# Performance work log

Hardware: AMD Instinct MI355X
Metric: run time of the kernel (lower is better)

Reference implementation:

```python
import jax, jax.numpy as jnp
import numpy as np

B, L, H, E = 2, 2048, 16, 64  # S == L (causal self-attention), D == E


def setup_inputs() -> dict:
    key = jax.random.key(0)
    kq, kk, kv, ks = jax.random.split(key, 4)
    queries = jax.random.normal(kq, (B, L, H, E), dtype=jnp.float32)
    keys = jax.random.normal(kk, (B, L, H, E), dtype=jnp.float32)
    values = jax.random.normal(kv, (B, L, H, E), dtype=jnp.float32)
    # TriangularCausalMask: True above the diagonal -> masked out
    attn_mask = jnp.broadcast_to(
        jnp.triu(jnp.ones((L, L), dtype=bool), k=1)[None, None], (B, 1, L, L)
    )
    init_score = jax.random.uniform(ks, (B, L, L), dtype=jnp.float32)
    return {
        "queries": queries,
        "keys": keys,
        "values": values,
        "attn_mask": attn_mask,
        "init_score": init_score,
    }


def reference(queries, keys, values, attn_mask, init_score):
    # queries: [B,L,H,E], keys: [B,S,H,E], values: [B,S,H,D]
    E_ = queries.shape[-1]
    scale = 1.0 / np.sqrt(E_).astype(np.float32)
    # scores: [B,H,L,S]
    scores = jnp.einsum('blhe,bshe->bhls', queries, keys)
    scores = jnp.where(attn_mask, -jnp.inf, scores)
    A = jax.nn.softmax(scale * scores, axis=-1)  # dropout p=0 -> identity
    # post-softmax bias, broadcast over heads
    A = A + 0.1 * init_score[:, None, :, :]
    # V: [B,L,H,D]
    V = jnp.einsum('bhls,bshd->blhd', A, values)
    return V
```

## Files before the change

kernel.cpp:

```cpp
#include <hip/hip_runtime.h>
#include <hip/hip_bf16.h>
#include <math.h>

#define BB 2
#define LL 2048
#define HH 16
#define EE 64
#define LOG2E 1.44269504089f

typedef __attribute__((ext_vector_type(8))) short short8;
typedef __attribute__((ext_vector_type(4))) float floatx4;
typedef unsigned int u32;

union S8 { short8 v; u32 u[4]; ushort4 q[2]; };

__device__ inline u32 pkbf(float lo, float hi) {
    union { __hip_bfloat162 h; u32 u; } c;
    c.h = __float22bfloat162_rn(make_float2(lo, hi));
    return c.u;
}

__device__ inline ushort4 cvt4(float4 v) {
    union { __hip_bfloat162 h; u32 u; } a, b;
    a.h = __float22bfloat162_rn(make_float2(v.x, v.y));
    b.h = __float22bfloat162_rn(make_float2(v.z, v.w));
    ushort4 r;
    r.x = (unsigned short)(a.u & 0xffffu);
    r.y = (unsigned short)(a.u >> 16);
    r.z = (unsigned short)(b.u & 0xffffu);
    r.w = (unsigned short)(b.u >> 16);
    return r;
}

__device__ inline short8 pack8(float4 a, float4 b) {
    S8 s; s.q[0] = cvt4(a); s.q[1] = cvt4(b); return s.v;
}

__device__ inline void async16(unsigned short* lds, const unsigned short* g) {
    __builtin_amdgcn_global_load_lds(
        (const __attribute__((address_space(1))) u32*)g,
        (__attribute__((address_space(3))) u32*)lds, 16, 0, 0);
}

__global__ __launch_bounds__(256) void prepass(
    const float* __restrict__ k, const float* __restrict__ v,
    const float* __restrict__ isc, unsigned short* __restrict__ kb,
    unsigned short* __restrict__ vt, unsigned short* __restrict__ isb)
{
    const int bid = blockIdx.x;
    const int t = threadIdx.x;
    if (bid < 1024) {
        #pragma unroll
        for (int it = 0; it < 2; ++it) {
            int idx = bid * 512 + it * 256 + t;
            const float4* src = (const float4*)k + idx * 2;
            float4 a = src[0], c = src[1];
            int e8 = idx & 7, h = (idx >> 3) & 15, l = (idx >> 7) & 2047, b = idx >> 18;
            *(short8*)&kb[(((b * 16 + h) * 2048 + l) * 64) + e8 * 8] = pack8(a, c);
        }
    } else if (bid < 2048) {
        const int ib = bid - 1024;
        #pragma unroll
        for (int it = 0; it < 4; ++it) {
            int idx = ib * 1024 + it * 256 + t;
            const float4* src = (const float4*)isc + idx * 2;
            float4 a = src[0], c = src[1];
            a.x *= 0.1f; a.y *= 0.1f; a.z *= 0.1f; a.w *= 0.1f;
            c.x *= 0.1f; c.y *= 0.1f; c.z *= 0.1f; c.w *= 0.1f;
            ((short8*)isb)[idx] = pack8(a, c);
        }
    } else {
        __shared__ float Tf[64][68];
        const int vb = bid - 2048;
        const int st = vb & 31, h = (vb >> 5) & 15, b = vb >> 9;
        const int s0 = st * 64;
        #pragma unroll
        for (int i = 0; i < 4; ++i) {
            int r = i * 16 + (t >> 4), c = (t & 15) * 4;
            float4 val = *(const float4*)(v + (((b * LL + s0 + r) * HH + h) * EE) + c);
            *(float4*)&Tf[r][c] = val;
        }
        __syncthreads();
        #pragma unroll
        for (int i = 0; i < 4; ++i) {
            int d = i * 16 + (t >> 4), s4 = (t & 15) * 4;
            float4 val = make_float4(Tf[s4 + 0][d], Tf[s4 + 1][d],
                                     Tf[s4 + 2][d], Tf[s4 + 3][d]);
            *(ushort4*)&vt[((b * 16 + h) * 64 + d) * 2048 + s0 + s4] = cvt4(val);
        }
    }
}

template <int MODE>
__device__ __forceinline__ void tile_step(
    const unsigned short* __restrict__ Ks, const unsigned short* __restrict__ Vs,
    const short8 qf[2], const short8 isf[2],
    floatx4 o_attn[4], floatx4 o_bias[4], float& lsum,
    int s0, int mbase, int wave, int lq, int ln, int lnl,
    int alo, int ahi, bool hisel)
{
    u32 pk[4][2];
    if (MODE < 2) {
        #pragma unroll
        for (int sb = 0; sb < 4; ++sb) {
            if (MODE == 1 && wave < sb) { pk[sb][0] = 0; pk[sb][1] = 0; continue; }
            short8 kf0 = *(const short8*)&Ks[(sb * 16 + ln) * 64 + ((lq ^ lnl) << 3)];
            short8 kf1 = *(const short8*)&Ks[(sb * 16 + ln) * 64 + (((4 + lq) ^ lnl) << 3)];
            floatx4 sa = {0.f, 0.f, 0.f, 0.f};
            sa = __builtin_amdgcn_mfma_f32_16x16x32_bf16(kf0, qf[0], sa, 0, 0, 0);
            sa = __builtin_amdgcn_mfma_f32_16x16x32_bf16(kf1, qf[1], sa, 0, 0, 0);
            float pv[4];
            #pragma unroll
            for (int r = 0; r < 4; ++r) {
                float t = sa[r];
                if (MODE == 1 && (s0 + sb * 16 + lq * 4 + r) > (mbase + ln)) t = -INFINITY;
                float p = exp2f(t);
                lsum += p;
                pv[r] = p;
            }
            pk[sb][0] = pkbf(pv[0], pv[1]);
            pk[sb][1] = pkbf(pv[2], pv[3]);
        }
    }
    #pragma unroll
    for (int kk = 0; kk < 2; ++kk) {
        short8 vf[4];
        #pragma unroll
        for (int db = 0; db < 4; ++db)
            vf[db] = *(const short8*)&Vs[(db * 16 + ln) * 64 + (((kk * 4 + lq) ^ lnl) << 3)];
        short8 af = isf[kk];
        #pragma unroll
        for (int db = 0; db < 4; ++db)
            o_bias[db] = __builtin_amdgcn_mfma_f32_16x16x32_bf16(af, vf[db], o_bias[db], 0, 0, 0);
        if (MODE < 2) {
            S8 pf;
            u32 a0 = (u32)__builtin_amdgcn_ds_bpermute(alo, (int)pk[kk * 2][0]);
            u32 b0 = (u32)__builtin_amdgcn_ds_bpermute(alo, (int)pk[kk * 2 + 1][0]);
            pf.u[0] = hisel ? b0 : a0;
            u32 a1 = (u32)__builtin_amdgcn_ds_bpermute(alo, (int)pk[kk * 2][1]);
            u32 b1 = (u32)__builtin_amdgcn_ds_bpermute(alo, (int)pk[kk * 2 + 1][1]);
            pf.u[1] = hisel ? b1 : a1;
            u32 a2 = (u32)__builtin_amdgcn_ds_bpermute(ahi, (int)pk[kk * 2][0]);
            u32 b2 = (u32)__builtin_amdgcn_ds_bpermute(ahi, (int)pk[kk * 2 + 1][0]);
            pf.u[2] = hisel ? b2 : a2;
            u32 a3 = (u32)__builtin_amdgcn_ds_bpermute(ahi, (int)pk[kk * 2][1]);
            u32 b3 = (u32)__builtin_amdgcn_ds_bpermute(ahi, (int)pk[kk * 2 + 1][1]);
            pf.u[3] = hisel ? b3 : a3;
            #pragma unroll
            for (int db = 0; db < 4; ++db)
                o_attn[db] = __builtin_amdgcn_mfma_f32_16x16x32_bf16(pf.v, vf[db], o_attn[db], 0, 0, 0);
        }
    }
}

__global__ __launch_bounds__(256, 4) void fused6(
    const float* __restrict__ q, const unsigned short* __restrict__ kb,
    const unsigned short* __restrict__ vt, const unsigned short* __restrict__ isb,
    float* __restrict__ out)
{
    __shared__ unsigned short Ks[2][64 * 64];
    __shared__ unsigned short Vs[2][64 * 64];

    const int tid = threadIdx.x, lane = tid & 63, wave = tid >> 6;
    const int lq = lane >> 4, ln = lane & 15, lnl = ln & 7;

    const int bid = blockIdx.x;
    const int h = bid & 15, b = (bid >> 4) & 1, g = bid >> 5;
    int qt;
    if (g < 8) qt = 31 - g;
    else if (g < 16) qt = g;
    else if (g < 24) qt = 39 - g;
    else qt = g - 24;
    const int q0 = qt * 64;
    const int mbase = q0 + wave * 16;

    short8 qf[2];
    {
        const float sc = 0.125f * LOG2E;
        const float* qrow = q + (((long)(b * LL + mbase + ln)) * HH + h) * EE;
        #pragma unroll
        for (int kk = 0; kk < 2; ++kk) {
            float4 a = *(const float4*)(qrow + kk * 32 + lq * 8);
            float4 c = *(const float4*)(qrow + kk * 32 + lq * 8 + 4);
            a.x *= sc; a.y *= sc; a.z *= sc; a.w *= sc;
            c.x *= sc; c.y *= sc; c.z *= sc; c.w *= sc;
            qf[kk] = pack8(a, c);
        }
    }

    const unsigned short* kbh = kb + (long)(b * HH + h) * (LL * EE);
    const unsigned short* vth = vt + (long)(b * HH + h) * (EE * LL);

    floatx4 o_attn[4], o_bias[4];
    #pragma unroll
    for (int db = 0; db < 4; ++db) {
        o_attn[db] = (floatx4){0.f, 0.f, 0.f, 0.f};
        o_bias[db] = (floatx4){0.f, 0.f, 0.f, 0.f};
    }
    float lsum = 0.f;

    const int rr = lane >> 3, jl = lane & 7;
    const int swz = (jl ^ rr) * 8;
    const unsigned short* ksrc0 = kbh + (wave * 16 + rr) * 64 + swz;
    const unsigned short* ksrc1 = kbh + (wave * 16 + 8 + rr) * 64 + swz;
    const unsigned short* vsrc0 = vth + (wave * 16 + rr) * LL + swz;
    const unsigned short* vsrc1 = vth + (wave * 16 + 8 + rr) * LL + swz;

    const unsigned short* isrow =
        isb + (long)(b * LL + q0 + wave * 16 + ln) * LL + lq * 8;

    const int alo = (((lq & 1) * 2) * 16 + ln) * 4;
    const int ahi = (((lq & 1) * 2 + 1) * 16 + ln) * 4;
    const bool hisel = (lq >= 2);

    auto issue = [&](int j) {
        const int s0 = j * 64, bsel = j & 1;
        if (j <= qt) {
            async16(&Ks[bsel][(wave * 16) * 64], ksrc0 + s0 * 64);
            async16(&Ks[bsel][(wave * 16 + 8) * 64], ksrc1 + s0 * 64);
        }
        async16(&Vs[bsel][(wave * 16) * 64], vsrc0 + s0);
        async16(&Vs[bsel][(wave * 16 + 8) * 64], vsrc1 + s0);
    };

    short8 isf[2], isfn[2];
    auto ldnext = [&](int j, short8* dst) {
        int jc = j < 32 ? j : 31;
        dst[0] = *(const short8*)(isrow + jc * 64);
        dst[1] = *(const short8*)(isrow + jc * 64 + 32);
    };

    ldnext(0, isf);
    issue(0);
    for (int j = 0; j < qt; ++j) {
        __syncthreads();
        issue(j + 1);
        ldnext(j + 1, isfn);
        tile_step<0>(Ks[j & 1], Vs[j & 1], qf, isf, o_attn, o_bias, lsum,
                     j * 64, mbase, wave, lq, ln, lnl, alo, ahi, hisel);
        isf[0] = isfn[0]; isf[1] = isfn[1];
    }
    {
        __syncthreads();
        if (qt < 31) issue(qt + 1);
        ldnext(qt + 1, isfn);
        tile_step<1>(Ks[qt & 1], Vs[qt & 1], qf, isf, o_attn, o_bias, lsum,
                     q0, mbase, wave, lq, ln, lnl, alo, ahi, hisel);
        isf[0] = isfn[0]; isf[1] = isfn[1];
    }
    for (int j = qt + 1; j < 32; ++j) {
        __syncthreads();
        if (j < 31) issue(j + 1);
        ldnext(j + 1, isfn);
        tile_step<2>(Vs[j & 1], Vs[j & 1], qf, isf, o_attn, o_bias, lsum,
                     j * 64, mbase, wave, lq, ln, lnl, alo, ahi, hisel);
        isf[0] = isfn[0]; isf[1] = isfn[1];
    }

    float s = lsum;
    s += __shfl_xor(s, 16);
    s += __shfl_xor(s, 32);
    #pragma unroll
    for (int r = 0; r < 4; ++r) {
        float inv = 1.0f / __shfl(s, lq * 4 + r);
        int m = mbase + lq * 4 + r;
        float* ob = out + (((long)(b * LL + m)) * HH + h) * EE;
        #pragma unroll
        for (int db = 0; db < 4; ++db)
            ob[db * 16 + ln] = o_attn[db][r] * inv + o_bias[db][r];
    }
}

extern "C" void kernel_launch(void* const* d_in, const int* in_sizes, int n_in,
                              void* d_out, int out_size, void* d_ws, size_t ws_size,
                              hipStream_t stream) {
    (void)in_sizes; (void)n_in; (void)out_size; (void)ws_size;
    const float* q   = (const float*)d_in[0];
    const float* k   = (const float*)d_in[1];
    const float* v   = (const float*)d_in[2];
    const float* isc = (const float*)d_in[4];
    float* out = (float*)d_out;

    unsigned short* kb  = (unsigned short*)d_ws;
    unsigned short* vt  = (unsigned short*)((char*)d_ws + (8u << 20));
    unsigned short* isb = (unsigned short*)((char*)d_ws + (16u << 20));

    prepass<<<dim3(3072), dim3(256), 0, stream>>>(k, v, isc, kb, vt, isb);
    fused6<<<dim3(1024), dim3(256), 0, stream>>>(q, kb, vt, isb, out);
}
```

Before: 197.9 us.

## Pair complementary query tiles per 512-thread block and read init_score directly in fp32

```diff
diff --git a/kernel.cpp b/kernel.cpp
--- a/kernel.cpp
+++ b/kernel.cpp
@@ -44,8 +44,7 @@
 
 __global__ __launch_bounds__(256) void prepass(
     const float* __restrict__ k, const float* __restrict__ v,
-    const float* __restrict__ isc, unsigned short* __restrict__ kb,
-    unsigned short* __restrict__ vt, unsigned short* __restrict__ isb)
+    unsigned short* __restrict__ kb, unsigned short* __restrict__ vt)
 {
     const int bid = blockIdx.x;
     const int t = threadIdx.x;
@@ -58,20 +57,9 @@
             int e8 = idx & 7, h = (idx >> 3) & 15, l = (idx >> 7) & 2047, b = idx >> 18;
             *(short8*)&kb[(((b * 16 + h) * 2048 + l) * 64) + e8 * 8] = pack8(a, c);
         }
-    } else if (bid < 2048) {
-        const int ib = bid - 1024;
-        #pragma unroll
-        for (int it = 0; it < 4; ++it) {
-            int idx = ib * 1024 + it * 256 + t;
-            const float4* src = (const float4*)isc + idx * 2;
-            float4 a = src[0], c = src[1];
-            a.x *= 0.1f; a.y *= 0.1f; a.z *= 0.1f; a.w *= 0.1f;
-            c.x *= 0.1f; c.y *= 0.1f; c.z *= 0.1f; c.w *= 0.1f;
-            ((short8*)isb)[idx] = pack8(a, c);
-        }
     } else {
         __shared__ float Tf[64][68];
-        const int vb = bid - 2048;
+        const int vb = bid - 1024;
         const int st = vb & 31, h = (vb >> 5) & 15, b = vb >> 9;
         const int s0 = st * 64;
         #pragma unroll
@@ -96,14 +84,14 @@
     const unsigned short* __restrict__ Ks, const unsigned short* __restrict__ Vs,
     const short8 qf[2], const short8 isf[2],
     floatx4 o_attn[4], floatx4 o_bias[4], float& lsum,
-    int s0, int mbase, int wave, int lq, int ln, int lnl,
+    int s0, int mbase, int w4, int lq, int ln, int lnl,
     int alo, int ahi, bool hisel)
 {
     u32 pk[4][2];
     if (MODE < 2) {
         #pragma unroll
         for (int sb = 0; sb < 4; ++sb) {
-            if (MODE == 1 && wave < sb) { pk[sb][0] = 0; pk[sb][1] = 0; continue; }
+            if (MODE == 1 && w4 < sb) { pk[sb][0] = 0; pk[sb][1] = 0; continue; }
             short8 kf0 = *(const short8*)&Ks[(sb * 16 + ln) * 64 + ((lq ^ lnl) << 3)];
             short8 kf1 = *(const short8*)&Ks[(sb * 16 + ln) * 64 + (((4 + lq) ^ lnl) << 3)];
             floatx4 sa = {0.f, 0.f, 0.f, 0.f};
@@ -153,26 +141,26 @@
     }
 }
 
-__global__ __launch_bounds__(256, 4) void fused6(
+__global__ __launch_bounds__(512, 4) void fused7(
     const float* __restrict__ q, const unsigned short* __restrict__ kb,
-    const unsigned short* __restrict__ vt, const unsigned short* __restrict__ isb,
+    const unsigned short* __restrict__ vt, const float* __restrict__ isc,
     float* __restrict__ out)
 {
     __shared__ unsigned short Ks[2][64 * 64];
     __shared__ unsigned short Vs[2][64 * 64];
 
     const int tid = threadIdx.x, lane = tid & 63, wave = tid >> 6;
+    const int w4 = wave & 3;
     const int lq = lane >> 4, ln = lane & 15, lnl = ln & 7;
 
     const int bid = blockIdx.x;
-    const int h = bid & 15, b = (bid >> 4) & 1, g = bid >> 5;
-    int qt;
-    if (g < 8) qt = 31 - g;
-    else if (g < 16) qt = g;
-    else if (g < 24) qt = 39 - g;
-    else qt = g - 24;
-    const int q0 = qt * 64;
-    const int mbase = q0 + wave * 16;
+    const int bh = bid & 31, h = bh & 15, b = bh >> 4;
+    const int pidx = (bid >> 5) & 7, half = bid >> 8;
+    const int qtA = half ? (31 - pidx) : (16 + pidx);
+    const int qtB = 31 - qtA;
+    const int myqt = __builtin_amdgcn_readfirstlane((wave >> 2) ? qtB : qtA);
+    const int q0 = myqt * 64;
+    const int mbase = q0 + w4 * 16;
 
     short8 qf[2];
     {
@@ -201,13 +189,10 @@
 
     const int rr = lane >> 3, jl = lane & 7;
     const int swz = (jl ^ rr) * 8;
-    const unsigned short* ksrc0 = kbh + (wave * 16 + rr) * 64 + swz;
-    const unsigned short* ksrc1 = kbh + (wave * 16 + 8 + rr) * 64 + swz;
-    const unsigned short* vsrc0 = vth + (wave * 16 + rr) * LL + swz;
-    const unsigned short* vsrc1 = vth + (wave * 16 + 8 + rr) * LL + swz;
-
-    const unsigned short* isrow =
-        isb + (long)(b * LL + q0 + wave * 16 + ln) * LL + lq * 8;
+    const unsigned short* ksrc = kbh + (wave * 8 + rr) * 64 + swz;
+    const unsigned short* vsrc = vth + (wave * 8 + rr) * LL + swz;
+
+    const float* isrow = isc + (long)(b * LL + q0 + w4 * 16 + ln) * LL + lq * 8;
 
     const int alo = (((lq & 1) * 2) * 16 + ln) * 4;
     const int ahi = (((lq & 1) * 2 + 1) * 16 + ln) * 4;
@@ -215,46 +200,48 @@
 
     auto issue = [&](int j) {
         const int s0 = j * 64, bsel = j & 1;
-        if (j <= qt) {
-            async16(&Ks[bsel][(wave * 16) * 64], ksrc0 + s0 * 64);
-            async16(&Ks[bsel][(wave * 16 + 8) * 64], ksrc1 + s0 * 64);
-        }
-        async16(&Vs[bsel][(wave * 16) * 64], vsrc0 + s0);
-        async16(&Vs[bsel][(wave * 16 + 8) * 64], vsrc1 + s0);
+        if (j <= qtA)
+            async16(&Ks[bsel][(wave * 8) * 64], ksrc + s0 * 64);
+        async16(&Vs[bsel][(wave * 8) * 64], vsrc + s0);
     };
 
-    short8 isf[2], isfn[2];
-    auto ldnext = [&](int j, short8* dst) {
+    float4 raw0, raw1, raw2, raw3;
+    auto ldraw = [&](int j) {
         int jc = j < 32 ? j : 31;
-        dst[0] = *(const short8*)(isrow + jc * 64);
-        dst[1] = *(const short8*)(isrow + jc * 64 + 32);
+        const float* p = isrow + jc * 64;
+        raw0 = *(const float4*)(p);
+        raw1 = *(const float4*)(p + 4);
+        raw2 = *(const float4*)(p + 32);
+        raw3 = *(const float4*)(p + 36);
     };
-
-    ldnext(0, isf);
+    short8 isf[2];
+    auto cvtis = [&]() {
+        float4 a = raw0, c = raw1, d = raw2, e = raw3;
+        a.x *= 0.1f; a.y *= 0.1f; a.z *= 0.1f; a.w *= 0.1f;
+        c.x *= 0.1f; c.y *= 0.1f; c.z *= 0.1f; c.w *= 0.1f;
+        d.x *= 0.1f; d.y *= 0.1f; d.z *= 0.1f; d.w *= 0.1f;
+        e.x *= 0.1f; e.y *= 0.1f; e.z *= 0.1f; e.w *= 0.1f;
+        isf[0] = pack8(a, c);
+        isf[1] = pack8(d, e);
+    };
+
+    ldraw(0); cvtis();
+    ldraw(1);
     issue(0);
-    for (int j = 0; j < qt; ++j) {
-        __syncthreads();
-        issue(j + 1);
-        ldnext(j + 1, isfn);
-        tile_step<0>(Ks[j & 1], Vs[j & 1], qf, isf, o_attn, o_bias, lsum,
-                     j * 64, mbase, wave, lq, ln, lnl, alo, ahi, hisel);
-        isf[0] = isfn[0]; isf[1] = isfn[1];
-    }
-    {
-        __syncthreads();
-        if (qt < 31) issue(qt + 1);
-        ldnext(qt + 1, isfn);
-        tile_step<1>(Ks[qt & 1], Vs[qt & 1], qf, isf, o_attn, o_bias, lsum,
-                     q0, mbase, wave, lq, ln, lnl, alo, ahi, hisel);
-        isf[0] = isfn[0]; isf[1] = isfn[1];
-    }
-    for (int j = qt + 1; j < 32; ++j) {
+    for (int j = 0; j < 32; ++j) {
         __syncthreads();
         if (j < 31) issue(j + 1);
-        ldnext(j + 1, isfn);
-        tile_step<2>(Vs[j & 1], Vs[j & 1], qf, isf, o_attn, o_bias, lsum,
-                     j * 64, mbase, wave, lq, ln, lnl, alo, ahi, hisel);
-        isf[0] = isfn[0]; isf[1] = isfn[1];
+        if (j < myqt)
+            tile_step<0>(Ks[j & 1], Vs[j & 1], qf, isf, o_attn, o_bias, lsum,
+                         j * 64, mbase, w4, lq, ln, lnl, alo, ahi, hisel);
+        else if (j == myqt)
+            tile_step<1>(Ks[j & 1], Vs[j & 1], qf, isf, o_attn, o_bias, lsum,
+                         q0, mbase, w4, lq, ln, lnl, alo, ahi, hisel);
+        else
+            tile_step<2>(Ks[j & 1], Vs[j & 1], qf, isf, o_attn, o_bias, lsum,
+                         j * 64, mbase, w4, lq, ln, lnl, alo, ahi, hisel);
+        cvtis();
+        ldraw(j + 2);
     }
 
     float s = lsum;
@@ -283,8 +270,7 @@
 
     unsigned short* kb  = (unsigned short*)d_ws;
     unsigned short* vt  = (unsigned short*)((char*)d_ws + (8u << 20));
-    unsigned short* isb = (unsigned short*)((char*)d_ws + (16u << 20));
-
-    prepass<<<dim3(3072), dim3(256), 0, stream>>>(k, v, isc, kb, vt, isb);
-    fused6<<<dim3(1024), dim3(256), 0, stream>>>(q, kb, vt, isb, out);
-}
+
+    prepass<<<dim3(2048), dim3(256), 0, stream>>>(k, v, kb, vt);
+    fused7<<<dim3(512), dim3(512), 0, stream>>>(q, kb, vt, isc, out);
+}
```

After: 385.5 us. 94.8% more time.

## Pre-swizzle K/V into MFMA fragment layout and load directly to registers

Applied to the files above, without the earlier changes.

```diff
diff --git a/kernel.cpp b/kernel.cpp
--- a/kernel.cpp
+++ b/kernel.cpp
@@ -36,30 +36,60 @@
     S8 s; s.q[0] = cvt4(a); s.q[1] = cvt4(b); return s.v;
 }
 
-__device__ inline void async16(unsigned short* lds, const unsigned short* g) {
-    __builtin_amdgcn_global_load_lds(
-        (const __attribute__((address_space(1))) u32*)g,
-        (__attribute__((address_space(3))) u32*)lds, 16, 0, 0);
-}
-
 __global__ __launch_bounds__(256) void prepass(
     const float* __restrict__ k, const float* __restrict__ v,
-    const float* __restrict__ isc, unsigned short* __restrict__ kb,
-    unsigned short* __restrict__ vt, unsigned short* __restrict__ isb)
+    const float* __restrict__ isc, unsigned short* __restrict__ kfrag,
+    unsigned short* __restrict__ vfrag, unsigned short* __restrict__ isb)
 {
     const int bid = blockIdx.x;
     const int t = threadIdx.x;
-    if (bid < 1024) {
-        #pragma unroll
-        for (int it = 0; it < 2; ++it) {
-            int idx = bid * 512 + it * 256 + t;
-            const float4* src = (const float4*)k + idx * 2;
-            float4 a = src[0], c = src[1];
-            int e8 = idx & 7, h = (idx >> 3) & 15, l = (idx >> 7) & 2047, b = idx >> 18;
-            *(short8*)&kb[(((b * 16 + h) * 2048 + l) * 64) + e8 * 8] = pack8(a, c);
-        }
-    } else if (bid < 2048) {
-        const int ib = bid - 1024;
+    if (bid < 2048) {
+        __shared__ unsigned short TL[64][72];
+        const bool isK = bid < 1024;
+        const int vb = bid & 1023;
+        const int j = vb & 31, h = (vb >> 5) & 15, b = vb >> 9;
+        const float* src = (isK ? k : v) + ((long)(b * LL + j * 64) * HH + h) * EE;
+        {
+            int r = t >> 2, c0 = (t & 3) * 16;
+            const float* p = src + (long)r * (HH * EE) + c0;
+            float4 f0 = *(const float4*)(p);
+            float4 f1 = *(const float4*)(p + 4);
+            float4 f2 = *(const float4*)(p + 8);
+            float4 f3 = *(const float4*)(p + 12);
+            *(ushort4*)&TL[r][c0]      = cvt4(f0);
+            *(ushort4*)&TL[r][c0 + 4]  = cvt4(f1);
+            *(ushort4*)&TL[r][c0 + 8]  = cvt4(f2);
+            *(ushort4*)&TL[r][c0 + 12] = cvt4(f3);
+        }
+        __syncthreads();
+        if (isK) {
+            unsigned short* outp = kfrag + ((long)(b * 16 + h) * 32 + j) * 4096;
+            #pragma unroll
+            for (int i = 0; i < 2; ++i) {
+                int slot = t * 2 + i;
+                int fid = slot >> 6, lane = slot & 63;
+                int sb = fid >> 1, kk = fid & 1;
+                int lnn = lane & 15, lqq = lane >> 4;
+                *(short8*)(outp + slot * 8) =
+                    *(const short8*)&TL[sb * 16 + lnn][kk * 32 + lqq * 8];
+            }
+        } else {
+            unsigned short* outp = vfrag + ((long)(b * 16 + h) * 32 + j) * 4096;
+            #pragma unroll
+            for (int i = 0; i < 2; ++i) {
+                int slot = t * 2 + i;
+                int fid = slot >> 6, lane = slot & 63;
+                int kk = fid >> 2, db = fid & 3;
+                int lnn = lane & 15, lqq = lane >> 4;
+                union { short8 v8; unsigned short us[8]; } g;
+                #pragma unroll
+                for (int jj = 0; jj < 8; ++jj)
+                    g.us[jj] = TL[kk * 32 + lqq * 8 + jj][db * 16 + lnn];
+                *(short8*)(outp + slot * 8) = g.v8;
+            }
+        }
+    } else {
+        const int ib = bid - 2048;
         #pragma unroll
         for (int it = 0; it < 4; ++it) {
             int idx = ib * 1024 + it * 256 + t;
@@ -69,69 +99,47 @@
             c.x *= 0.1f; c.y *= 0.1f; c.z *= 0.1f; c.w *= 0.1f;
             ((short8*)isb)[idx] = pack8(a, c);
         }
-    } else {
-        __shared__ float Tf[64][68];
-        const int vb = bid - 2048;
-        const int st = vb & 31, h = (vb >> 5) & 15, b = vb >> 9;
-        const int s0 = st * 64;
-        #pragma unroll
-        for (int i = 0; i < 4; ++i) {
-            int r = i * 16 + (t >> 4), c = (t & 15) * 4;
-            float4 val = *(const float4*)(v + (((b * LL + s0 + r) * HH + h) * EE) + c);
-            *(float4*)&Tf[r][c] = val;
-        }
-        __syncthreads();
-        #pragma unroll
-        for (int i = 0; i < 4; ++i) {
-            int d = i * 16 + (t >> 4), s4 = (t & 15) * 4;
-            float4 val = make_float4(Tf[s4 + 0][d], Tf[s4 + 1][d],
-                                     Tf[s4 + 2][d], Tf[s4 + 3][d]);
-            *(ushort4*)&vt[((b * 16 + h) * 64 + d) * 2048 + s0 + s4] = cvt4(val);
-        }
     }
 }
 
 template <int MODE>
 __device__ __forceinline__ void tile_step(
-    const unsigned short* __restrict__ Ks, const unsigned short* __restrict__ Vs,
-    const short8 qf[2], const short8 isf[2],
-    floatx4 o_attn[4], floatx4 o_bias[4], float& lsum,
-    int s0, int mbase, int wave, int lq, int ln, int lnl,
+    short8 kf[8], short8 vf[8], const short8 qf[2], const short8 isf[2],
+    const short8 ones, floatx4 o_attn[4], floatx4 o_bias[4], floatx4& o_sum,
+    const unsigned short* kfn, const unsigned short* vfn,
+    int s0, int mbase, int w4, int lq, int ln,
     int alo, int ahi, bool hisel)
 {
     u32 pk[4][2];
     if (MODE < 2) {
         #pragma unroll
         for (int sb = 0; sb < 4; ++sb) {
-            if (MODE == 1 && wave < sb) { pk[sb][0] = 0; pk[sb][1] = 0; continue; }
-            short8 kf0 = *(const short8*)&Ks[(sb * 16 + ln) * 64 + ((lq ^ lnl) << 3)];
-            short8 kf1 = *(const short8*)&Ks[(sb * 16 + ln) * 64 + (((4 + lq) ^ lnl) << 3)];
+            if (MODE == 1 && w4 < sb) { pk[sb][0] = 0; pk[sb][1] = 0; continue; }
             floatx4 sa = {0.f, 0.f, 0.f, 0.f};
-            sa = __builtin_amdgcn_mfma_f32_16x16x32_bf16(kf0, qf[0], sa, 0, 0, 0);
-            sa = __builtin_amdgcn_mfma_f32_16x16x32_bf16(kf1, qf[1], sa, 0, 0, 0);
+            sa = __builtin_amdgcn_mfma_f32_16x16x32_bf16(kf[sb * 2 + 0], qf[0], sa, 0, 0, 0);
+            sa = __builtin_amdgcn_mfma_f32_16x16x32_bf16(kf[sb * 2 + 1], qf[1], sa, 0, 0, 0);
             float pv[4];
             #pragma unroll
             for (int r = 0; r < 4; ++r) {
                 float t = sa[r];
                 if (MODE == 1 && (s0 + sb * 16 + lq * 4 + r) > (mbase + ln)) t = -INFINITY;
-                float p = exp2f(t);
-                lsum += p;
-                pv[r] = p;
+                pv[r] = exp2f(t);
             }
             pk[sb][0] = pkbf(pv[0], pv[1]);
             pk[sb][1] = pkbf(pv[2], pv[3]);
         }
+        if (kfn) {
+            #pragma unroll
+            for (int f = 0; f < 8; ++f)
+                kf[f] = *(const short8*)(kfn + f * 512);
+        }
     }
     #pragma unroll
     for (int kk = 0; kk < 2; ++kk) {
-        short8 vf[4];
+        short8 af = isf[kk];
         #pragma unroll
         for (int db = 0; db < 4; ++db)
-            vf[db] = *(const short8*)&Vs[(db * 16 + ln) * 64 + (((kk * 4 + lq) ^ lnl) << 3)];
-        short8 af = isf[kk];
-        #pragma unroll
-        for (int db = 0; db < 4; ++db)
-            o_bias[db] = __builtin_amdgcn_mfma_f32_16x16x32_bf16(af, vf[db], o_bias[db], 0, 0, 0);
+            o_bias[db] = __builtin_amdgcn_mfma_f32_16x16x32_bf16(af, vf[kk * 4 + db], o_bias[db], 0, 0, 0);
         if (MODE < 2) {
             S8 pf;
             u32 a0 = (u32)__builtin_amdgcn_ds_bpermute(alo, (int)pk[kk * 2][0]);
@@ -146,23 +154,26 @@
             u32 a3 = (u32)__builtin_amdgcn_ds_bpermute(ahi, (int)pk[kk * 2][1]);
             u32 b3 = (u32)__builtin_amdgcn_ds_bpermute(ahi, (int)pk[kk * 2 + 1][1]);
             pf.u[3] = hisel ? b3 : a3;
+            o_sum = __builtin_amdgcn_mfma_f32_16x16x32_bf16(pf.v, ones, o_sum, 0, 0, 0);
             #pragma unroll
             for (int db = 0; db < 4; ++db)
-                o_attn[db] = __builtin_amdgcn_mfma_f32_16x16x32_bf16(pf.v, vf[db], o_attn[db], 0, 0, 0);
-        }
-    }
-}
-
-__global__ __launch_bounds__(256, 4) void fused6(
-    const float* __restrict__ q, const unsigned short* __restrict__ kb,
-    const unsigned short* __restrict__ vt, const unsigned short* __restrict__ isb,
+                o_attn[db] = __builtin_amdgcn_mfma_f32_16x16x32_bf16(pf.v, vf[kk * 4 + db], o_attn[db], 0, 0, 0);
+        }
+    }
+    if (vfn) {
+        #pragma unroll
+        for (int f = 0; f < 8; ++f)
+            vf[f] = *(const short8*)(vfn + f * 512);
+    }
+}
+
+__global__ __launch_bounds__(256, 3) void fused8(
+    const float* __restrict__ q, const unsigned short* __restrict__ kfrag,
+    const unsigned short* __restrict__ vfrag, const unsigned short* __restrict__ isb,
     float* __restrict__ out)
 {
-    __shared__ unsigned short Ks[2][64 * 64];
-    __shared__ unsigned short Vs[2][64 * 64];
-
     const int tid = threadIdx.x, lane = tid & 63, wave = tid >> 6;
-    const int lq = lane >> 4, ln = lane & 15, lnl = ln & 7;
+    const int lq = lane >> 4, ln = lane & 15;
 
     const int bid = blockIdx.x;
     const int h = bid & 15, b = (bid >> 4) & 1, g = bid >> 5;
@@ -188,8 +199,11 @@
         }
     }
 
-    const unsigned short* kbh = kb + (long)(b * HH + h) * (LL * EE);
-    const unsigned short* vth = vt + (long)(b * HH + h) * (EE * LL);
+    const unsigned short* kfh = kfrag + (long)(b * 16 + h) * 32 * 4096;
+    const unsigned short* vfh = vfrag + (long)(b * 16 + h) * 32 * 4096;
+    const unsigned short* isrow =
+        isb + (long)(b * LL + q0 + wave * 16 + ln) * LL + lq * 8;
+    const int l8 = lane * 8;
 
     floatx4 o_attn[4], o_bias[4];
     #pragma unroll
@@ -197,72 +211,52 @@
         o_attn[db] = (floatx4){0.f, 0.f, 0.f, 0.f};
         o_bias[db] = (floatx4){0.f, 0.f, 0.f, 0.f};
     }
-    float lsum = 0.f;
-
-    const int rr = lane >> 3, jl = lane & 7;
-    const int swz = (jl ^ rr) * 8;
-    const unsigned short* ksrc0 = kbh + (wave * 16 + rr) * 64 + swz;
-    const unsigned short* ksrc1 = kbh + (wave * 16 + 8 + rr) * 64 + swz;
-    const unsigned short* vsrc0 = vth + (wave * 16 + rr) * LL + swz;
-    const unsigned short* vsrc1 = vth + (wave * 16 + 8 + rr) * LL + swz;
-
-    const unsigned short* isrow =
-        isb + (long)(b * LL + q0 + wave * 16 + ln) * LL + lq * 8;
+    floatx4 o_sum = (floatx4){0.f, 0.f, 0.f, 0.f};
+    const short8 ones = {(short)0x3F80, (short)0x3F80, (short)0x3F80, (short)0x3F80,
+                         (short)0x3F80, (short)0x3F80, (short)0x3F80, (short)0x3F80};
 
     const int alo = (((lq & 1) * 2) * 16 + ln) * 4;
     const int ahi = (((lq & 1) * 2 + 1) * 16 + ln) * 4;
     const bool hisel = (lq >= 2);
 
-    auto issue = [&](int j) {
-        const int s0 = j * 64, bsel = j & 1;
-        if (j <= qt) {
-            async16(&Ks[bsel][(wave * 16) * 64], ksrc0 + s0 * 64);
-            async16(&Ks[bsel][(wave * 16 + 8) * 64], ksrc1 + s0 * 64);
-        }
-        async16(&Vs[bsel][(wave * 16) * 64], vsrc0 + s0);
-        async16(&Vs[bsel][(wave * 16 + 8) * 64], vsrc1 + s0);
-    };
-
-    short8 isf[2], isfn[2];
-    auto ldnext = [&](int j, short8* dst) {
-        int jc = j < 32 ? j : 31;
-        dst[0] = *(const short8*)(isrow + jc * 64);
-        dst[1] = *(const short8*)(isrow + jc * 64 + 32);
-    };
-
-    ldnext(0, isf);
-    issue(0);
+    short8 kf[8], vf[8], isf[2], isfn[2];
+    #pragma unroll
+    for (int f = 0; f < 8; ++f) kf[f] = *(const short8*)(kfh + f * 512 + l8);
+    #pragma unroll
+    for (int f = 0; f < 8; ++f) vf[f] = *(const short8*)(vfh + f * 512 + l8);
+    isf[0] = *(const short8*)(isrow);
+    isf[1] = *(const short8*)(isrow + 32);
+
     for (int j = 0; j < qt; ++j) {
-        __syncthreads();
-        issue(j + 1);
-        ldnext(j + 1, isfn);
-        tile_step<0>(Ks[j & 1], Vs[j & 1], qf, isf, o_attn, o_bias, lsum,
-                     j * 64, mbase, wave, lq, ln, lnl, alo, ahi, hisel);
+        isfn[0] = *(const short8*)(isrow + (j + 1) * 64);
+        isfn[1] = *(const short8*)(isrow + (j + 1) * 64 + 32);
+        tile_step<0>(kf, vf, qf, isf, ones, o_attn, o_bias, o_sum,
+                     kfh + (j + 1) * 4096 + l8, vfh + (j + 1) * 4096 + l8,
+                     j * 64, mbase, wave, lq, ln, alo, ahi, hisel);
         isf[0] = isfn[0]; isf[1] = isfn[1];
     }
     {
-        __syncthreads();
-        if (qt < 31) issue(qt + 1);
-        ldnext(qt + 1, isfn);
-        tile_step<1>(Ks[qt & 1], Vs[qt & 1], qf, isf, o_attn, o_bias, lsum,
-                     q0, mbase, wave, lq, ln, lnl, alo, ahi, hisel);
+        int jn = qt + 1 < 32 ? qt + 1 : 31;
+        isfn[0] = *(const short8*)(isrow + jn * 64);
+        isfn[1] = *(const short8*)(isrow + jn * 64 + 32);
+        tile_step<1>(kf, vf, qf, isf, ones, o_attn, o_bias, o_sum,
+                     nullptr, (qt < 31) ? vfh + (qt + 1) * 4096 + l8 : nullptr,
+                     q0, mbase, wave, lq, ln, alo, ahi, hisel);
         isf[0] = isfn[0]; isf[1] = isfn[1];
     }
     for (int j = qt + 1; j < 32; ++j) {
-        __syncthreads();
-        if (j < 31) issue(j + 1);
-        ldnext(j + 1, isfn);
-        tile_step<2>(Vs[j & 1], Vs[j & 1], qf, isf, o_attn, o_bias, lsum,
-                     j * 64, mbase, wave, lq, ln, lnl, alo, ahi, hisel);
+        int jn = j + 1 < 32 ? j + 1 : 31;
+        isfn[0] = *(const short8*)(isrow + jn * 64);
+        isfn[1] = *(const short8*)(isrow + jn * 64 + 32);
+        tile_step<2>(kf, vf, qf, isf, ones, o_attn, o_bias, o_sum,
+                     nullptr, (j < 31) ? vfh + (j + 1) * 4096 + l8 : nullptr,
+                     j * 64, mbase, wave, lq, ln, alo, ahi, hisel);
         isf[0] = isfn[0]; isf[1] = isfn[1];
     }
 
-    float s = lsum;
-    s += __shfl_xor(s, 16);
-    s += __shfl_xor(s, 32);
     #pragma unroll
     for (int r = 0; r < 4; ++r) {
-        float inv = 1.0f / __shfl(s, lq * 4 + r);
+        float inv = 1.0f / o_sum[r];
         int m = mbase + lq * 4 + r;
         float* ob = out + (((long)(b * LL + m)) * HH + h) * EE;
         #pragma unroll
@@ -281,10 +275,10 @@
     const float* isc = (const float*)d_in[4];
     float* out = (float*)d_out;
 
-    unsigned short* kb  = (unsigned short*)d_ws;
-    unsigned short* vt  = (unsigned short*)((char*)d_ws + (8u << 20));
-    unsigned short* isb = (unsigned short*)((char*)d_ws + (16u << 20));
-
-    prepass<<<dim3(3072), dim3(256), 0, stream>>>(k, v, isc, kb, vt, isb);
-    fused6<<<dim3(1024), dim3(256), 0, stream>>>(q, kb, vt, isb, out);
-}
+    unsigned short* kfrag = (unsigned short*)d_ws;
+    unsigned short* vfrag = (unsigned short*)((char*)d_ws + (8u << 20));
+    unsigned short* isb   = (unsigned short*)((char*)d_ws + (16u << 20));
+
+    prepass<<<dim3(3072), dim3(256), 0, stream>>>(k, v, isc, kfrag, vfrag, isb);
+    fused8<<<dim3(1024), dim3(256), 0, stream>>>(q, kfrag, vfrag, isb, out);
+}
```

New measurement: 229.4 us. 1.16x slower.

## Triple-buffer K/V/bias tiles via async LDS loads with explicit vmcnt waits

Applied to the files above, without the earlier changes.

```diff
diff --git a/kernel.cpp b/kernel.cpp
--- a/kernel.cpp
+++ b/kernel.cpp
@@ -59,7 +59,26 @@
             *(short8*)&kb[(((b * 16 + h) * 2048 + l) * 64) + e8 * 8] = pack8(a, c);
         }
     } else if (bid < 2048) {
-        const int ib = bid - 1024;
+        __shared__ float Tf[64][68];
+        const int vb = bid - 1024;
+        const int st = vb & 31, h = (vb >> 5) & 15, b = vb >> 9;
+        const int s0 = st * 64;
+        #pragma unroll
+        for (int i = 0; i < 4; ++i) {
+            int r = i * 16 + (t >> 4), c = (t & 15) * 4;
+            float4 val = *(const float4*)(v + (((b * LL + s0 + r) * HH + h) * EE) + c);
+            *(float4*)&Tf[r][c] = val;
+        }
+        __syncthreads();
+        #pragma unroll
+        for (int i = 0; i < 4; ++i) {
+            int d = i * 16 + (t >> 4), s4 = (t & 15) * 4;
+            float4 val = make_float4(Tf[s4 + 0][d], Tf[s4 + 1][d],
+                                     Tf[s4 + 2][d], Tf[s4 + 3][d]);
+            *(ushort4*)&vt[((b * 16 + h) * 64 + d) * 2048 + s0 + s4] = cvt4(val);
+        }
+    } else {
+        const int ib = bid - 2048;
         #pragma unroll
         for (int it = 0; it < 4; ++it) {
             int idx = ib * 1024 + it * 256 + t;
@@ -69,54 +88,36 @@
             c.x *= 0.1f; c.y *= 0.1f; c.z *= 0.1f; c.w *= 0.1f;
             ((short8*)isb)[idx] = pack8(a, c);
         }
-    } else {
-        __shared__ float Tf[64][68];
-        const int vb = bid - 2048;
-        const int st = vb & 31, h = (vb >> 5) & 15, b = vb >> 9;
-        const int s0 = st * 64;
-        #pragma unroll
-        for (int i = 0; i < 4; ++i) {
-            int r = i * 16 + (t >> 4), c = (t & 15) * 4;
-            float4 val = *(const float4*)(v + (((b * LL + s0 + r) * HH + h) * EE) + c);
-            *(float4*)&Tf[r][c] = val;
-        }
-        __syncthreads();
-        #pragma unroll
-        for (int i = 0; i < 4; ++i) {
-            int d = i * 16 + (t >> 4), s4 = (t & 15) * 4;
-            float4 val = make_float4(Tf[s4 + 0][d], Tf[s4 + 1][d],
-                                     Tf[s4 + 2][d], Tf[s4 + 3][d]);
-            *(ushort4*)&vt[((b * 16 + h) * 64 + d) * 2048 + s0 + s4] = cvt4(val);
-        }
     }
 }
 
 template <int MODE>
 __device__ __forceinline__ void tile_step(
     const unsigned short* __restrict__ Ks, const unsigned short* __restrict__ Vs,
-    const short8 qf[2], const short8 isf[2],
-    floatx4 o_attn[4], floatx4 o_bias[4], float& lsum,
-    int s0, int mbase, int wave, int lq, int ln, int lnl,
+    const unsigned short* __restrict__ Is,
+    const short8 qf[2], const short8 ones,
+    floatx4 o_attn[4], floatx4 o_bias[4], floatx4& o_sum,
+    int s0, int mbase, int w4, int lq, int ln, int lnl,
     int alo, int ahi, bool hisel)
 {
     u32 pk[4][2];
     if (MODE < 2) {
         #pragma unroll
         for (int sb = 0; sb < 4; ++sb) {
-            if (MODE == 1 && wave < sb) { pk[sb][0] = 0; pk[sb][1] = 0; continue; }
+            if (MODE == 1 && w4 < sb) { pk[sb][0] = 0; pk[sb][1] = 0; continue; }
             short8 kf0 = *(const short8*)&Ks[(sb * 16 + ln) * 64 + ((lq ^ lnl) << 3)];
             short8 kf1 = *(const short8*)&Ks[(sb * 16 + ln) * 64 + (((4 + lq) ^ lnl) << 3)];
             floatx4 sa = {0.f, 0.f, 0.f, 0.f};
+            __builtin_amdgcn_s_setprio(1);
             sa = __builtin_amdgcn_mfma_f32_16x16x32_bf16(kf0, qf[0], sa, 0, 0, 0);
             sa = __builtin_amdgcn_mfma_f32_16x16x32_bf16(kf1, qf[1], sa, 0, 0, 0);
+            __builtin_amdgcn_s_setprio(0);
             float pv[4];
             #pragma unroll
             for (int r = 0; r < 4; ++r) {
                 float t = sa[r];
                 if (MODE == 1 && (s0 + sb * 16 + lq * 4 + r) > (mbase + ln)) t = -INFINITY;
-                float p = exp2f(t);
-                lsum += p;
-                pv[r] = p;
+                pv[r] = exp2f(t);
             }
             pk[sb][0] = pkbf(pv[0], pv[1]);
             pk[sb][1] = pkbf(pv[2], pv[3]);
@@ -128,10 +129,12 @@
         #pragma unroll
         for (int db = 0; db < 4; ++db)
             vf[db] = *(const short8*)&Vs[(db * 16 + ln) * 64 + (((kk * 4 + lq) ^ lnl) << 3)];
-        short8 af = isf[kk];
+        short8 af = *(const short8*)&Is[(w4 * 16 + ln) * 64 + (((kk * 4 + lq) ^ lnl) << 3)];
+        __builtin_amdgcn_s_setprio(1);
         #pragma unroll
         for (int db = 0; db < 4; ++db)
             o_bias[db] = __builtin_amdgcn_mfma_f32_16x16x32_bf16(af, vf[db], o_bias[db], 0, 0, 0);
+        __builtin_amdgcn_s_setprio(0);
         if (MODE < 2) {
             S8 pf;
             u32 a0 = (u32)__builtin_amdgcn_ds_bpermute(alo, (int)pk[kk * 2][0]);
@@ -146,31 +149,32 @@
             u32 a3 = (u32)__builtin_amdgcn_ds_bpermute(ahi, (int)pk[kk * 2][1]);
             u32 b3 = (u32)__builtin_amdgcn_ds_bpermute(ahi, (int)pk[kk * 2 + 1][1]);
             pf.u[3] = hisel ? b3 : a3;
+            __builtin_amdgcn_s_setprio(1);
+            o_sum = __builtin_amdgcn_mfma_f32_16x16x32_bf16(pf.v, ones, o_sum, 0, 0, 0);
             #pragma unroll
             for (int db = 0; db < 4; ++db)
                 o_attn[db] = __builtin_amdgcn_mfma_f32_16x16x32_bf16(pf.v, vf[db], o_attn[db], 0, 0, 0);
-        }
-    }
-}
-
-__global__ __launch_bounds__(256, 4) void fused6(
+            __builtin_amdgcn_s_setprio(0);
+        }
+    }
+}
+
+__global__ __launch_bounds__(256, 2) void fused9(
     const float* __restrict__ q, const unsigned short* __restrict__ kb,
     const unsigned short* __restrict__ vt, const unsigned short* __restrict__ isb,
     float* __restrict__ out)
 {
-    __shared__ unsigned short Ks[2][64 * 64];
-    __shared__ unsigned short Vs[2][64 * 64];
+    __shared__ unsigned short Ks[3][64 * 64];
+    __shared__ unsigned short Vs[3][64 * 64];
+    __shared__ unsigned short Is[3][64 * 64];
 
     const int tid = threadIdx.x, lane = tid & 63, wave = tid >> 6;
     const int lq = lane >> 4, ln = lane & 15, lnl = ln & 7;
 
     const int bid = blockIdx.x;
     const int h = bid & 15, b = (bid >> 4) & 1, g = bid >> 5;
-    int qt;
-    if (g < 8) qt = 31 - g;
-    else if (g < 16) qt = g;
-    else if (g < 24) qt = 39 - g;
-    else qt = g - 24;
+    const int gh = g >> 1;
+    const int qt = (g & 1) ? gh : 31 - gh;
     const int q0 = qt * 64;
     const int mbase = q0 + wave * 16;
 
@@ -197,7 +201,9 @@
         o_attn[db] = (floatx4){0.f, 0.f, 0.f, 0.f};
         o_bias[db] = (floatx4){0.f, 0.f, 0.f, 0.f};
     }
-    float lsum = 0.f;
+    floatx4 o_sum = (floatx4){0.f, 0.f, 0.f, 0.f};
+    const short8 ones = {(short)0x3F80, (short)0x3F80, (short)0x3F80, (short)0x3F80,
+                         (short)0x3F80, (short)0x3F80, (short)0x3F80, (short)0x3F80};
 
     const int rr = lane >> 3, jl = lane & 7;
     const int swz = (jl ^ rr) * 8;
@@ -205,64 +211,53 @@
     const unsigned short* ksrc1 = kbh + (wave * 16 + 8 + rr) * 64 + swz;
     const unsigned short* vsrc0 = vth + (wave * 16 + rr) * LL + swz;
     const unsigned short* vsrc1 = vth + (wave * 16 + 8 + rr) * LL + swz;
-
-    const unsigned short* isrow =
-        isb + (long)(b * LL + q0 + wave * 16 + ln) * LL + lq * 8;
+    const unsigned short* isrc0 = isb + (long)(b * LL + q0 + wave * 16 + rr) * LL + swz;
+    const unsigned short* isrc1 = isrc0 + 8 * LL;
 
     const int alo = (((lq & 1) * 2) * 16 + ln) * 4;
     const int ahi = (((lq & 1) * 2 + 1) * 16 + ln) * 4;
     const bool hisel = (lq >= 2);
 
-    auto issue = [&](int j) {
-        const int s0 = j * 64, bsel = j & 1;
-        if (j <= qt) {
-            async16(&Ks[bsel][(wave * 16) * 64], ksrc0 + s0 * 64);
-            async16(&Ks[bsel][(wave * 16 + 8) * 64], ksrc1 + s0 * 64);
-        }
-        async16(&Vs[bsel][(wave * 16) * 64], vsrc0 + s0);
-        async16(&Vs[bsel][(wave * 16 + 8) * 64], vsrc1 + s0);
+    auto issue = [&](int t) {
+        const int s0 = t * 64;
+        const int m3 = t % 3;
+        if (t <= qt) {
+            async16(&Ks[m3][(wave * 16) * 64], ksrc0 + s0 * 64);
+            async16(&Ks[m3][(wave * 16 + 8) * 64], ksrc1 + s0 * 64);
+        }
+        async16(&Vs[m3][(wave * 16) * 64], vsrc0 + s0);
+        async16(&Vs[m3][(wave * 16 + 8) * 64], vsrc1 + s0);
+        async16(&Is[m3][(wave * 16) * 64], isrc0 + s0);
+        async16(&Is[m3][(wave * 16 + 8) * 64], isrc1 + s0);
     };
 
-    short8 isf[2], isfn[2];
-    auto ldnext = [&](int j, short8* dst) {
-        int jc = j < 32 ? j : 31;
-        dst[0] = *(const short8*)(isrow + jc * 64);
-        dst[1] = *(const short8*)(isrow + jc * 64 + 32);
-    };
-
-    ldnext(0, isf);
     issue(0);
-    for (int j = 0; j < qt; ++j) {
-        __syncthreads();
-        issue(j + 1);
-        ldnext(j + 1, isfn);
-        tile_step<0>(Ks[j & 1], Vs[j & 1], qf, isf, o_attn, o_bias, lsum,
-                     j * 64, mbase, wave, lq, ln, lnl, alo, ahi, hisel);
-        isf[0] = isfn[0]; isf[1] = isfn[1];
-    }
-    {
-        __syncthreads();
-        if (qt < 31) issue(qt + 1);
-        ldnext(qt + 1, isfn);
-        tile_step<1>(Ks[qt & 1], Vs[qt & 1], qf, isf, o_attn, o_bias, lsum,
-                     q0, mbase, wave, lq, ln, lnl, alo, ahi, hisel);
-        isf[0] = isfn[0]; isf[1] = isfn[1];
-    }
-    for (int j = qt + 1; j < 32; ++j) {
-        __syncthreads();
-        if (j < 31) issue(j + 1);
-        ldnext(j + 1, isfn);
-        tile_step<2>(Vs[j & 1], Vs[j & 1], qf, isf, o_attn, o_bias, lsum,
-                     j * 64, mbase, wave, lq, ln, lnl, alo, ahi, hisel);
-        isf[0] = isfn[0]; isf[1] = isfn[1];
-    }
-
-    float s = lsum;
-    s += __shfl_xor(s, 16);
-    s += __shfl_xor(s, 32);
+    issue(1);
+    for (int j = 0; j < 32; ++j) {
+        if (j == 31)
+            asm volatile("s_waitcnt vmcnt(0)" ::: "memory");
+        else if (j + 1 <= qt)
+            asm volatile("s_waitcnt vmcnt(6)" ::: "memory");
+        else
+            asm volatile("s_waitcnt vmcnt(4)" ::: "memory");
+        __builtin_amdgcn_s_barrier();
+        __builtin_amdgcn_sched_barrier(0);
+        if (j + 2 < 32) issue(j + 2);
+        const int m3 = j % 3;
+        if (j < qt)
+            tile_step<0>(Ks[m3], Vs[m3], Is[m3], qf, ones, o_attn, o_bias, o_sum,
+                         j * 64, mbase, wave, lq, ln, lnl, alo, ahi, hisel);
+        else if (j == qt)
+            tile_step<1>(Ks[m3], Vs[m3], Is[m3], qf, ones, o_attn, o_bias, o_sum,
+                         q0, mbase, wave, lq, ln, lnl, alo, ahi, hisel);
+        else
+            tile_step<2>(Ks[m3], Vs[m3], Is[m3], qf, ones, o_attn, o_bias, o_sum,
+                         j * 64, mbase, wave, lq, ln, lnl, alo, ahi, hisel);
+    }
+
     #pragma unroll
     for (int r = 0; r < 4; ++r) {
-        float inv = 1.0f / __shfl(s, lq * 4 + r);
+        float inv = 1.0f / o_sum[r];
         int m = mbase + lq * 4 + r;
         float* ob = out + (((long)(b * LL + m)) * HH + h) * EE;
         #pragma unroll
@@ -286,5 +281,5 @@
     unsigned short* isb = (unsigned short*)((char*)d_ws + (16u << 20));
 
     prepass<<<dim3(3072), dim3(256), 0, stream>>>(k, v, isc, kb, vt, isb);
-    fused6<<<dim3(1024), dim3(256), 0, stream>>>(q, kb, vt, isb, out);
-}
+    fused9<<<dim3(1024), dim3(256), 0, stream>>>(q, kb, vt, isb, out);
+}
```

After: 224.1 us. +13.2%, slower.
